# Optimization experiments

Hardware: AMD Instinct MI355X
Metric: run time of the kernel (lower is better)

## Reference

```python
import jax, jax.numpy as jnp
import numpy as np

N_HEADS = 4
M = 16            # n_points (neighbors kept per voxel)
DIST = 4          # manhattan distance threshold
D_MODEL = 128
D_FFN = 256
D_CHL = 64
GRID = 96         # spatial_shape per axis
LN_EPS = 1e-5
BN_EPS = 1e-3


def setup_inputs() -> dict:
    key = jax.random.key(0)
    ks = jax.random.split(key, 24)
    N = 8192
    w = lambda k, s: jax.random.normal(k, s, jnp.float32) * 0.02
    z = lambda d: jnp.zeros((d,), jnp.float32)
    o = lambda d: jnp.ones((d,), jnp.float32)
    return {
        "features": jax.random.normal(ks[0], (N, D_CHL), jnp.float32),
        "coords": jax.random.randint(ks[1], (N, 3), 0, GRID, jnp.int32),
        "pe_w1": w(ks[2], (3, D_MODEL // 2)), "pe_b1": z(D_MODEL // 2),
        "pe_w2": w(ks[3], (D_MODEL // 2, D_MODEL)), "pe_b2": z(D_MODEL),
        "in_w": w(ks[4], (D_CHL, D_MODEL)), "in_b": z(D_MODEL),
        "q_w": w(ks[5], (D_MODEL, D_MODEL)), "q_b": z(D_MODEL),
        "k_w": w(ks[6], (D_MODEL, D_MODEL)), "k_b": z(D_MODEL),
        "v_w": w(ks[7], (D_MODEL, D_MODEL)), "v_b": z(D_MODEL),
        "o_w": w(ks[8], (D_MODEL, D_MODEL)), "o_b": z(D_MODEL),
        "n1_g": o(D_MODEL), "n1_b": z(D_MODEL),
        "l1_w": w(ks[9], (D_MODEL, D_FFN)), "l1_b": z(D_FFN),
        "l2_w": w(ks[10], (D_FFN, D_MODEL)), "l2_b": z(D_MODEL),
        "n3_g": o(D_MODEL), "n3_b": z(D_MODEL),
        "fu_w": w(ks[11], (D_MODEL + D_CHL, D_CHL)), "fu_b": z(D_CHL),
        "bn_g": o(D_CHL), "bn_b": z(D_CHL),
    }


def _layernorm(x, g, b):
    mu = jnp.mean(x, -1, keepdims=True)
    var = jnp.mean(jnp.square(x - mu), -1, keepdims=True)
    return (x - mu) * jax.lax.rsqrt(var + LN_EPS) * g + b


def reference(features, coords, pe_w1, pe_b1, pe_w2, pe_b2, in_w, in_b,
              q_w, q_b, k_w, k_b, v_w, v_b, o_w, o_b, n1_g, n1_b,
              l1_w, l1_b, l2_w, l2_b, n3_g, n3_b, fu_w, fu_b, bn_g, bn_b):
    N = features.shape[0]
    hd = D_MODEL // N_HEADS
    ci = coords.astype(jnp.float32)
    # input projection + dynamic learnable positional encoding
    src = features @ in_w + in_b
    vc = ci / (GRID - 1.0)
    src = src + (jax.nn.relu(vc @ pe_w1 + pe_b1) @ pe_w2 + pe_b2)
    # pairwise manhattan distances; accumulate per coordinate to avoid [N,N,3]
    dist = jnp.zeros((N, N), jnp.float32)
    for d in range(3):
        dist = dist + jnp.abs(ci[:, d, None] - ci[None, :, d])
    dist = jnp.where(dist <= DIST, dist, jnp.inf)
    neg_top, idx = jax.lax.top_k(-dist, M)          # [N, M]
    valid = neg_top != -jnp.inf
    # gather neighbor features; invalid slots are zero (as in torch)
    nb = jnp.where(valid[:, :, None], src[jnp.where(valid, idx, 0)], 0.0)  # [N,M,D]
    # cross-attention: query is neighbor 0 (self). NOTE: faithful raw .view
    # reshape of [N,M,D] -> [N,H,M,hd] (interleaves neighbor/head axes as torch does)
    q = (nb[:, :1] @ q_w + q_b).reshape(N, N_HEADS, 1, hd)
    k = (nb @ k_w + k_b).reshape(N, N_HEADS, M, hd)
    v = (nb @ v_w + v_b).reshape(N, N_HEADS, M, hd)
    scores = jnp.einsum('nhqd,nhkd->nhqk', q, k) / jnp.sqrt(jnp.float32(D_MODEL))
    attn = jax.nn.softmax(scores, axis=-1)
    head_out = jnp.einsum('nhqk,nhkd->nhqd', attn, v).reshape(N, D_MODEL)
    out = head_out @ o_w + o_b
    tgt = _layernorm(src + out, n1_g, n1_b)
    # FFN
    tgt2 = jax.nn.relu(tgt @ l1_w + l1_b) @ l2_w + l2_b
    tgt = _layernorm(tgt + tgt2, n3_g, n3_b)
    # EnhancedFusion: concat -> linear -> batchnorm (train-mode stats) -> relu
    fused = jnp.concatenate([features, tgt], axis=1) @ fu_w + fu_b
    mu = jnp.mean(fused, 0)
    var = jnp.var(fused, 0)
    fused = (fused - mu) * jax.lax.rsqrt(var + BN_EPS) * bn_g + bn_b
    return jax.nn.relu(fused)
```

## Files before the change

### kernel.cpp

```cpp
#include <hip/hip_runtime.h>

#define DEVFN __device__ __forceinline__

DEVFN float relu(float x) { return x < 0.f ? 0.f : x; }

__global__ __launch_bounds__(256, 4) void ka_pre_cst(
    const float* __restrict__ features, const int* __restrict__ coords,
    const float* __restrict__ pe_w1, const float* __restrict__ pe_b1,
    const float* __restrict__ pe_w2, const float* __restrict__ pe_b2,
    const float* __restrict__ in_w, const float* __restrict__ in_b,
    const float* __restrict__ q_w, const float* __restrict__ k_w,
    const float* __restrict__ v_w,
    float* __restrict__ src,
    float* __restrict__ qs, float* __restrict__ ks, float* __restrict__ vs,
    int* __restrict__ nbr, float* __restrict__ bnAcc, int N)
{
    __shared__ float sF[512];
    __shared__ float sH[512];
    __shared__ float S[1024];
    __shared__ int   sC[24];
    __shared__ int cnt[16];
    __shared__ int lst[16 * 64];
    __shared__ int outL[256];

    const int tid = threadIdx.x;
    const int bx = blockIdx.x;
    const int role_nbr = (bx % 3) == 2;

    if (role_nbr) {
        const int nb = bx / 3;
        const int q0 = nb * 16;
        if (nb == 0 && tid < 128) bnAcc[tid] = 0.f;
        if (tid < 16) cnt[tid] = 0;
        outL[tid] = -1;
        __syncthreads();
        int qx[16], qy[16], qz[16];
#pragma unroll
        for (int q = 0; q < 16; ++q) {
            qx[q] = coords[(q0 + q) * 3 + 0];
            qy[q] = coords[(q0 + q) * 3 + 1];
            qz[q] = coords[(q0 + q) * 3 + 2];
        }
        for (int cd = tid; cd < N; cd += 256) {
            int cx = coords[cd * 3 + 0];
            int cy = coords[cd * 3 + 1];
            int cz = coords[cd * 3 + 2];
#pragma unroll
            for (int q = 0; q < 16; ++q) {
                int dx = cx - qx[q]; dx = dx < 0 ? -dx : dx;
                int dy = cy - qy[q]; dy = dy < 0 ? -dy : dy;
                int dz = cz - qz[q]; dz = dz < 0 ? -dz : dz;
                int d = dx + dy + dz;
                if (d <= 4) {
                    int s = atomicAdd(&cnt[q], 1);
                    if (s < 64) lst[q * 64 + s] = (d << 13) | cd;
                }
            }
        }
        __syncthreads();
        {
            const int q = tid >> 4, t = tid & 15;
            int n = cnt[q]; if (n > 64) n = 64;
            for (int e = t; e < n; e += 16) {
                int key = lst[q * 64 + e];
                int rank = 0;
                for (int j = 0; j < n; ++j) rank += (lst[q * 64 + j] < key) ? 1 : 0;
                if (rank < 16) outL[q * 16 + rank] = key & 8191;
            }
        }
        __syncthreads();
        {
            const int q = tid >> 4, t = tid & 15;
            nbr[(q0 + q) * 16 + t] = outL[q * 16 + t];
        }
        return;
    }

    const int sb = (bx / 3) * 2 + (bx % 3);
    const int r0 = sb * 8;
    if (tid < 24) sC[tid] = coords[r0 * 3 + tid];
    for (int i = tid; i < 512; i += 256) sF[i] = features[r0 * 64 + i];
    __syncthreads();
    for (int i = tid; i < 512; i += 256) {
        int r = i >> 6, t = i & 63;
        float v0 = sC[r * 3 + 0] * (1.f / 95.f);
        float v1 = sC[r * 3 + 1] * (1.f / 95.f);
        float v2 = sC[r * 3 + 2] * (1.f / 95.f);
        float h = v0 * pe_w1[t] + v1 * pe_w1[64 + t] + v2 * pe_w1[128 + t] + pe_b1[t];
        sH[i] = relu(h);
    }
    __syncthreads();
    const int c = tid & 127, rh = tid >> 7;
    {
        float acc[4];
        const float base = in_b[c] + pe_b2[c];
#pragma unroll
        for (int r = 0; r < 4; ++r) acc[r] = base;
        for (int j = 0; j < 64; ++j) {
            float w1 = in_w[j * 128 + c];
            float w2 = pe_w2[j * 128 + c];
#pragma unroll
            for (int r = 0; r < 4; ++r) {
                int rr = rh * 4 + r;
                acc[r] += sF[rr * 64 + j] * w1 + sH[rr * 64 + j] * w2;
            }
        }
#pragma unroll
        for (int r = 0; r < 4; ++r) {
            src[(r0 + rh * 4 + r) * 128 + c] = acc[r];
            S[(rh * 4 + r) * 128 + c] = acc[r];
        }
    }
    __syncthreads();
    {
        float aq[4], ak[4], av[4];
#pragma unroll
        for (int r = 0; r < 4; ++r) { aq[r] = 0.f; ak[r] = 0.f; av[r] = 0.f; }
        for (int k4 = 0; k4 < 32; ++k4) {
            float wq0 = q_w[(k4 * 4 + 0) * 128 + c];
            float wq1 = q_w[(k4 * 4 + 1) * 128 + c];
            float wq2 = q_w[(k4 * 4 + 2) * 128 + c];
            float wq3 = q_w[(k4 * 4 + 3) * 128 + c];
            float wk0 = k_w[(k4 * 4 + 0) * 128 + c];
            float wk1 = k_w[(k4 * 4 + 1) * 128 + c];
            float wk2 = k_w[(k4 * 4 + 2) * 128 + c];
            float wk3 = k_w[(k4 * 4 + 3) * 128 + c];
            float wv0 = v_w[(k4 * 4 + 0) * 128 + c];
            float wv1 = v_w[(k4 * 4 + 1) * 128 + c];
            float wv2 = v_w[(k4 * 4 + 2) * 128 + c];
            float wv3 = v_w[(k4 * 4 + 3) * 128 + c];
#pragma unroll
            for (int r = 0; r < 4; ++r) {
                float4 s = *(const float4*)(&S[(rh * 4 + r) * 128 + k4 * 4]);
                aq[r] += s.x * wq0 + s.y * wq1 + s.z * wq2 + s.w * wq3;
                ak[r] += s.x * wk0 + s.y * wk1 + s.z * wk2 + s.w * wk3;
                av[r] += s.x * wv0 + s.y * wv1 + s.z * wv2 + s.w * wv3;
            }
        }
#pragma unroll
        for (int r = 0; r < 4; ++r) {
            qs[(r0 + rh * 4 + r) * 128 + c] = aq[r];
            ks[(r0 + rh * 4 + r) * 128 + c] = ak[r];
            vs[(r0 + rh * 4 + r) * 128 + c] = av[r];
        }
    }
}

DEVFN void ln_rows8(float* Cb, const float* __restrict__ g,
                    const float* __restrict__ b, int tid)
{
    const int r = tid >> 5, l = tid & 31;
    float x[4]; float s = 0.f, s2 = 0.f;
#pragma unroll
    for (int i = 0; i < 4; ++i) {
        x[i] = Cb[r * 128 + l * 4 + i];
        s += x[i]; s2 += x[i] * x[i];
    }
#pragma unroll
    for (int o = 1; o < 32; o <<= 1) { s += __shfl_xor(s, o); s2 += __shfl_xor(s2, o); }
    float mu = s * (1.f / 128.f);
    float var = s2 * (1.f / 128.f) - mu * mu;
    float rstd = rsqrtf(var + 1e-5f);
#pragma unroll
    for (int i = 0; i < 4; ++i) {
        int cc = l * 4 + i;
        Cb[r * 128 + cc] = (x[i] - mu) * rstd * g[cc] + b[cc];
    }
}

__global__ __launch_bounds__(256, 4) void k4_main_cst(
    const float* __restrict__ features, const float* __restrict__ src,
    const float* __restrict__ qs, const float* __restrict__ ks, const float* __restrict__ vs,
    const int* __restrict__ nbr,
    const float* __restrict__ q_b, const float* __restrict__ k_b,
    const float* __restrict__ v_b,
    const float* __restrict__ o_w, const float* __restrict__ o_b,
    const float* __restrict__ n1_g, const float* __restrict__ n1_b,
    const float* __restrict__ l1_w, const float* __restrict__ l1_b,
    const float* __restrict__ l2_w, const float* __restrict__ l2_b,
    const float* __restrict__ n3_g, const float* __restrict__ n3_b,
    const float* __restrict__ fu_w, const float* __restrict__ fu_b,
    float* __restrict__ fused, float* __restrict__ bnSum, float* __restrict__ bnSq)
{
    __shared__ float A[1024];
    __shared__ float Bt[1024];
    __shared__ float C[1024];
    __shared__ float Q[1024];
    __shared__ float H[2048];
    __shared__ float SC[512];
    __shared__ float F[512];
    __shared__ __align__(16) float bK[128], bV[128];
    __shared__ int idxL[128];
    const int tid = threadIdx.x;
    const int r0 = blockIdx.x * 8;

    for (int i = tid; i < 1024; i += 256) A[i] = src[r0 * 128 + i];
    for (int i = tid; i < 512; i += 256) F[i] = features[r0 * 64 + i];
    if (tid < 128) {
        idxL[tid] = nbr[r0 * 16 + tid];
        bK[tid] = k_b[tid]; bV[tid] = v_b[tid];
    }
    __syncthreads();
    {
        int r = tid >> 5, cg = tid & 31;
        int i0 = idxL[r * 16];
        float4 qv = make_float4(0.f, 0.f, 0.f, 0.f);
        if (i0 >= 0) qv = *(const float4*)(qs + i0 * 128 + cg * 4);
        float4 qb = *(const float4*)(q_b + cg * 4);
        qv.x += qb.x; qv.y += qb.y; qv.z += qb.z; qv.w += qb.w;
        *(float4*)(&Q[r * 128 + cg * 4]) = qv;
    }
    __syncthreads();

    const int ar = tid >> 5, ah = (tid >> 3) & 3, ag = tid & 7;
    {
#pragma unroll
        for (int jj = 0; jj < 2; ++jj) {
            int j = ag + jj * 8;
            int j4 = j >> 2, ch = j & 3;
            int id = idxL[ar * 16 + ah * 4 + j4];
            float s = 0.f;
#pragma unroll
            for (int c4 = 0; c4 < 8; ++c4) {
                float4 qv = *(const float4*)(&Q[ar * 128 + ah * 32 + c4 * 4]);
                float4 kb = *(const float4*)(&bK[ch * 32 + c4 * 4]);
                float4 kv = make_float4(0.f, 0.f, 0.f, 0.f);
                if (id >= 0) kv = *(const float4*)(ks + id * 128 + ch * 32 + c4 * 4);
                s += qv.x * (kv.x + kb.x) + qv.y * (kv.y + kb.y)
                   + qv.z * (kv.z + kb.z) + qv.w * (kv.w + kb.w);
            }
            SC[ar * 64 + ah * 16 + j] = s * 0.08838834764831845f;
        }
    }
    __syncthreads();

    {
        float p[16];
        float mx = -3.4e38f;
#pragma unroll
        for (int j = 0; j < 16; ++j) { p[j] = SC[ar * 64 + ah * 16 + j]; mx = fmaxf(mx, p[j]); }
        float sum = 0.f;
#pragma unroll
        for (int j = 0; j < 16; ++j) { p[j] = __expf(p[j] - mx); sum += p[j]; }
        float inv = 1.f / sum;
        float4 acc = make_float4(0.f, 0.f, 0.f, 0.f);
#pragma unroll
        for (int j = 0; j < 16; ++j) {
            int j4 = j >> 2, ch = j & 3;
            int id = idxL[ar * 16 + ah * 4 + j4];
            float4 vb = *(const float4*)(&bV[ch * 32 + ag * 4]);
            float4 vv = make_float4(0.f, 0.f, 0.f, 0.f);
            if (id >= 0) vv = *(const float4*)(vs + id * 128 + ch * 32 + ag * 4);
            float w = p[j] * inv;
            acc.x += w * (vv.x + vb.x); acc.y += w * (vv.y + vb.y);
            acc.z += w * (vv.z + vb.z); acc.w += w * (vv.w + vb.w);
        }
        *(float4*)(&Bt[ar * 128 + ah * 32 + ag * 4]) = acc;
    }
    __syncthreads();

    {
        const int c = tid & 127, kh = tid >> 7;
        float acc[8];
#pragma unroll
        for (int r = 0; r < 8; ++r) acc[r] = 0.f;
        const float* wp = o_w + kh * 64 * 128 + c;
        for (int k4 = 0; k4 < 16; ++k4) {
            float w0 = wp[(k4 * 4 + 0) * 128];
            float w1 = wp[(k4 * 4 + 1) * 128];
            float w2 = wp[(k4 * 4 + 2) * 128];
            float w3 = wp[(k4 * 4 + 3) * 128];
#pragma unroll
            for (int r = 0; r < 8; ++r) {
                float4 t = *(const float4*)(&Bt[r * 128 + kh * 64 + k4 * 4]);
                acc[r] += t.x * w0 + t.y * w1 + t.z * w2 + t.w * w3;
            }
        }
#pragma unroll
        for (int r = 0; r < 8; ++r) H[kh * 1024 + r * 128 + c] = acc[r];
    }
    __syncthreads();
    for (int i = tid; i < 1024; i += 256) {
        int c = i & 127;
        C[i] = A[i] + o_b[c] + H[i] + H[1024 + i];
    }
    __syncthreads();
    ln_rows8(C, n1_g, n1_b, tid);
    __syncthreads();

    {
        const int f = tid;
        float acc[8];
#pragma unroll
        for (int r = 0; r < 8; ++r) acc[r] = 0.f;
        for (int k4 = 0; k4 < 32; ++k4) {
            float w0 = l1_w[(k4 * 4 + 0) * 256 + f];
            float w1 = l1_w[(k4 * 4 + 1) * 256 + f];
            float w2 = l1_w[(k4 * 4 + 2) * 256 + f];
            float w3 = l1_w[(k4 * 4 + 3) * 256 + f];
#pragma unroll
            for (int r = 0; r < 8; ++r) {
                float4 t = *(const float4*)(&C[r * 128 + k4 * 4]);
                acc[r] += t.x * w0 + t.y * w1 + t.z * w2 + t.w * w3;
            }
        }
        const float bb = l1_b[f];
#pragma unroll
        for (int r = 0; r < 8; ++r) H[r * 256 + f] = relu(acc[r] + bb);
    }
    __syncthreads();

    {
        const int c = tid & 127, kh = tid >> 7;
        float acc[8];
#pragma unroll
        for (int r = 0; r < 8; ++r) acc[r] = 0.f;
        const float* wp = l2_w + kh * 128 * 128 + c;
        for (int k4 = 0; k4 < 32; ++k4) {
            float w0 = wp[(k4 * 4 + 0) * 128];
            float w1 = wp[(k4 * 4 + 1) * 128];
            float w2 = wp[(k4 * 4 + 2) * 128];
            float w3 = wp[(k4 * 4 + 3) * 128];
#pragma unroll
            for (int r = 0; r < 8; ++r) {
                float4 t = *(const float4*)(&H[r * 256 + kh * 128 + k4 * 4]);
                acc[r] += t.x * w0 + t.y * w1 + t.z * w2 + t.w * w3;
            }
        }
        float* P = kh ? Bt : A;
#pragma unroll
        for (int r = 0; r < 8; ++r) P[r * 128 + c] = acc[r];
    }
    __syncthreads();
    for (int i = tid; i < 1024; i += 256) {
        int c = i & 127;
        C[i] += l2_b[c] + A[i] + Bt[i];
    }
    __syncthreads();
    ln_rows8(C, n3_g, n3_b, tid);
    __syncthreads();

    {
        const int c = tid & 63, rg = tid >> 6;
        float acc[2];
        const float fb = fu_b[c];
#pragma unroll
        for (int r = 0; r < 2; ++r) acc[r] = fb;
        for (int j4 = 0; j4 < 16; ++j4) {
            float w0 = fu_w[(j4 * 4 + 0) * 64 + c];
            float w1 = fu_w[(j4 * 4 + 1) * 64 + c];
            float w2 = fu_w[(j4 * 4 + 2) * 64 + c];
            float w3 = fu_w[(j4 * 4 + 3) * 64 + c];
#pragma unroll
            for (int r = 0; r < 2; ++r) {
                float4 t = *(const float4*)(&F[(rg * 2 + r) * 64 + j4 * 4]);
                acc[r] += t.x * w0 + t.y * w1 + t.z * w2 + t.w * w3;
            }
        }
        for (int j4 = 0; j4 < 32; ++j4) {
            float w0 = fu_w[(64 + j4 * 4 + 0) * 64 + c];
            float w1 = fu_w[(64 + j4 * 4 + 1) * 64 + c];
            float w2 = fu_w[(64 + j4 * 4 + 2) * 64 + c];
            float w3 = fu_w[(64 + j4 * 4 + 3) * 64 + c];
#pragma unroll
            for (int r = 0; r < 2; ++r) {
                float4 t = *(const float4*)(&C[(rg * 2 + r) * 128 + j4 * 4]);
                acc[r] += t.x * w0 + t.y * w1 + t.z * w2 + t.w * w3;
            }
        }
#pragma unroll
        for (int r = 0; r < 2; ++r) {
            int row = rg * 2 + r;
            float v = acc[r];
            fused[(r0 + row) * 64 + c] = v;
            H[row * 64 + c] = v;
        }
    }
    __syncthreads();
    if (tid < 64) {
        float s = 0.f, s2 = 0.f;
#pragma unroll
        for (int r = 0; r < 8; ++r) { float x = H[r * 64 + tid]; s += x; s2 += x * x; }
        atomicAdd(&bnSum[tid], s);
        atomicAdd(&bnSq[tid], s2);
    }
}

__global__ __launch_bounds__(256) void k5_bn_cst(
    const float* __restrict__ fused, const float* __restrict__ bnSum,
    const float* __restrict__ bnSq,
    const float* __restrict__ g, const float* __restrict__ b,
    float* __restrict__ out, int N)
{
    const int total = N * 64;
    const float invN = 1.f / (float)N;
    for (int i = blockIdx.x * 256 + threadIdx.x; i < total; i += gridDim.x * 256) {
        int c = i & 63;
        float mu = bnSum[c] * invN;
        float var = bnSq[c] * invN - mu * mu;
        float x = fused[i];
        float y = (x - mu) * rsqrtf(var + 1e-3f) * g[c] + b[c];
        out[i] = relu(y);
    }
}

extern "C" void kernel_launch(void* const* d_in, const int* in_sizes, int n_in,
                              void* d_out, int out_size, void* d_ws, size_t ws_size,
                              hipStream_t stream)
{
    const float* features = (const float*)d_in[0];
    const int*   coords   = (const int*)d_in[1];
    const float* pe_w1 = (const float*)d_in[2];
    const float* pe_b1 = (const float*)d_in[3];
    const float* pe_w2 = (const float*)d_in[4];
    const float* pe_b2 = (const float*)d_in[5];
    const float* in_w  = (const float*)d_in[6];
    const float* in_b  = (const float*)d_in[7];
    const float* q_w   = (const float*)d_in[8];
    const float* q_b   = (const float*)d_in[9];
    const float* k_w   = (const float*)d_in[10];
    const float* k_b   = (const float*)d_in[11];
    const float* v_w   = (const float*)d_in[12];
    const float* v_b   = (const float*)d_in[13];
    const float* o_w   = (const float*)d_in[14];
    const float* o_b   = (const float*)d_in[15];
    const float* n1_g  = (const float*)d_in[16];
    const float* n1_b  = (const float*)d_in[17];
    const float* l1_w  = (const float*)d_in[18];
    const float* l1_b  = (const float*)d_in[19];
    const float* l2_w  = (const float*)d_in[20];
    const float* l2_b  = (const float*)d_in[21];
    const float* n3_g  = (const float*)d_in[22];
    const float* n3_b  = (const float*)d_in[23];
    const float* fu_w  = (const float*)d_in[24];
    const float* fu_b  = (const float*)d_in[25];
    const float* bn_g  = (const float*)d_in[26];
    const float* bn_b  = (const float*)d_in[27];

    const int N = in_sizes[0] / 64;

    float* src   = (float*)d_ws;
    float* qs    = src + (size_t)N * 128;
    float* ks    = qs  + (size_t)N * 128;
    float* vs    = ks  + (size_t)N * 128;
    float* fused = vs  + (size_t)N * 128;
    int*   nbr    = (int*)(fused + (size_t)N * 64);
    float* bnSum  = (float*)(nbr + (size_t)N * 16);
    float* bnSq   = bnSum + 64;

    ka_pre_cst<<<N / 8 + N / 16, 256, 0, stream>>>(features, coords,
                                                   pe_w1, pe_b1, pe_w2, pe_b2,
                                                   in_w, in_b, q_w, k_w, v_w,
                                                   src, qs, ks, vs, nbr, bnSum, N);
    k4_main_cst<<<N / 8, 256, 0, stream>>>(features, src, qs, ks, vs, nbr,
                                           q_b, k_b, v_b, o_w, o_b, n1_g, n1_b,
                                           l1_w, l1_b, l2_w, l2_b, n3_g, n3_b,
                                           fu_w, fu_b, fused, bnSum, bnSq);
    k5_bn_cst<<<512, 256, 0, stream>>>(fused, bnSum, bnSq, bn_g, bn_b,
                                       (float*)d_out, N);
}
```

Measured before the change: 218.2 us.

## Retile dense GEMMs in main kernel to 4-column register tiles with split-K

Rewrites the o_w, l1_w and l2_w matmuls in the main per-8-row kernel. Each thread now computes a 4-column by 2-or-4-row float4 tile with vectorised weight loads, and the K dimension is split across thread groups whose partial sums are reduced through shared memory. The bias, residual and ReLU epilogues are fused into that reduction, which removes the separate elementwise passes and their barriers. The goal is fewer scalar global weight loads and more register reuse per shared-memory read, at the cost of extra shared-memory partial buffers and serialised reduction steps. It also disables unrolling on the fusion linear loops.

```diff
diff --git a/kernel.cpp b/kernel.cpp
--- a/kernel.cpp
+++ b/kernel.cpp
@@ -168,6 +168,17 @@
     }
 }
 
+DEVFN void op4(float4& acc, const float4 a,
+               const float4 w0, const float4 w1, const float4 w2, const float4 w3)
+{
+    acc.x += a.x * w0.x + a.y * w1.x + a.z * w2.x + a.w * w3.x;
+    acc.y += a.x * w0.y + a.y * w1.y + a.z * w2.y + a.w * w3.y;
+    acc.z += a.x * w0.z + a.y * w1.z + a.z * w2.z + a.w * w3.z;
+    acc.w += a.x * w0.w + a.y * w1.w + a.z * w2.w + a.w * w3.w;
+}
+DEVFN float4 f4add(float4 a, float4 b)
+{ return make_float4(a.x + b.x, a.y + b.y, a.z + b.z, a.w + b.w); }
+
 __global__ __launch_bounds__(256, 4) void k4_main_cst(
     const float* __restrict__ features, const float* __restrict__ src,
     const float* __restrict__ qs, const float* __restrict__ ks, const float* __restrict__ vs,
@@ -182,13 +193,13 @@
     const float* __restrict__ fu_w, const float* __restrict__ fu_b,
     float* __restrict__ fused, float* __restrict__ bnSum, float* __restrict__ bnSq)
 {
-    __shared__ float A[1024];
-    __shared__ float Bt[1024];
-    __shared__ float C[1024];
-    __shared__ float Q[1024];
-    __shared__ float H[2048];
-    __shared__ float SC[512];
-    __shared__ float F[512];
+    __shared__ __align__(16) float A[1024];
+    __shared__ __align__(16) float Bt[1024];
+    __shared__ __align__(16) float C[1024];
+    __shared__ __align__(16) float Q[1024];
+    __shared__ __align__(16) float H[2048];
+    __shared__ __align__(16) float SC[512];
+    __shared__ __align__(16) float F[512];
     __shared__ __align__(16) float bK[128], bV[128];
     __shared__ int idxL[128];
     const int tid = threadIdx.x;
@@ -260,83 +271,149 @@
     __syncthreads();
 
     {
-        const int c = tid & 127, kh = tid >> 7;
-        float acc[8];
-#pragma unroll
-        for (int r = 0; r < 8; ++r) acc[r] = 0.f;
-        const float* wp = o_w + kh * 64 * 128 + c;
-        for (int k4 = 0; k4 < 16; ++k4) {
-            float w0 = wp[(k4 * 4 + 0) * 128];
-            float w1 = wp[(k4 * 4 + 1) * 128];
-            float w2 = wp[(k4 * 4 + 2) * 128];
-            float w3 = wp[(k4 * 4 + 3) * 128];
-#pragma unroll
-            for (int r = 0; r < 8; ++r) {
-                float4 t = *(const float4*)(&Bt[r * 128 + kh * 64 + k4 * 4]);
-                acc[r] += t.x * w0 + t.y * w1 + t.z * w2 + t.w * w3;
-            }
-        }
-#pragma unroll
-        for (int r = 0; r < 8; ++r) H[kh * 1024 + r * 128 + c] = acc[r];
-    }
-    __syncthreads();
-    for (int i = tid; i < 1024; i += 256) {
-        int c = i & 127;
-        C[i] = A[i] + o_b[c] + H[i] + H[1024 + i];
-    }
-    __syncthreads();
+        const int cg = tid & 31, rp = (tid >> 5) & 3, kh = tid >> 7;
+        const int c0 = cg * 4, r0l = rp * 2, k0 = kh * 64;
+        float4 ac0 = make_float4(0.f, 0.f, 0.f, 0.f);
+        float4 ac1 = make_float4(0.f, 0.f, 0.f, 0.f);
+#pragma unroll 1
+        for (int s = 0; s < 16; ++s) {
+            const int kk = k0 + s * 4;
+            const float* wp = o_w + kk * 128 + c0;
+            float4 w0 = *(const float4*)(wp);
+            float4 w1 = *(const float4*)(wp + 128);
+            float4 w2 = *(const float4*)(wp + 256);
+            float4 w3 = *(const float4*)(wp + 384);
+            float4 a0 = *(const float4*)(&Bt[(r0l + 0) * 128 + kk]);
+            float4 a1 = *(const float4*)(&Bt[(r0l + 1) * 128 + kk]);
+            op4(ac0, a0, w0, w1, w2, w3);
+            op4(ac1, a1, w0, w1, w2, w3);
+        }
+        if (kh) {
+            *(float4*)(&H[(r0l + 0) * 128 + c0]) = ac0;
+            *(float4*)(&H[(r0l + 1) * 128 + c0]) = ac1;
+        }
+        __syncthreads();
+        if (kh == 0) {
+            float4 ob = *(const float4*)(o_b + c0);
+#pragma unroll
+            for (int r = 0; r < 2; ++r) {
+                const int base = (r0l + r) * 128 + c0;
+                float4 av = *(const float4*)(&A[base]);
+                float4 ph = *(const float4*)(&H[base]);
+                float4 me = r ? ac1 : ac0;
+                float4 cv;
+                cv.x = av.x + ob.x + me.x + ph.x;
+                cv.y = av.y + ob.y + me.y + ph.y;
+                cv.z = av.z + ob.z + me.z + ph.z;
+                cv.w = av.w + ob.w + me.w + ph.w;
+                *(float4*)(&C[base]) = cv;
+            }
+        }
+        __syncthreads();
+    }
     ln_rows8(C, n1_g, n1_b, tid);
     __syncthreads();
 
     {
-        const int f = tid;
-        float acc[8];
-#pragma unroll
-        for (int r = 0; r < 8; ++r) acc[r] = 0.f;
-        for (int k4 = 0; k4 < 32; ++k4) {
-            float w0 = l1_w[(k4 * 4 + 0) * 256 + f];
-            float w1 = l1_w[(k4 * 4 + 1) * 256 + f];
-            float w2 = l1_w[(k4 * 4 + 2) * 256 + f];
-            float w3 = l1_w[(k4 * 4 + 3) * 256 + f];
-#pragma unroll
-            for (int r = 0; r < 8; ++r) {
-                float4 t = *(const float4*)(&C[r * 128 + k4 * 4]);
-                acc[r] += t.x * w0 + t.y * w1 + t.z * w2 + t.w * w3;
-            }
-        }
-        const float bb = l1_b[f];
-#pragma unroll
-        for (int r = 0; r < 8; ++r) H[r * 256 + f] = relu(acc[r] + bb);
-    }
-    __syncthreads();
-
-    {
-        const int c = tid & 127, kh = tid >> 7;
-        float acc[8];
-#pragma unroll
-        for (int r = 0; r < 8; ++r) acc[r] = 0.f;
-        const float* wp = l2_w + kh * 128 * 128 + c;
-        for (int k4 = 0; k4 < 32; ++k4) {
-            float w0 = wp[(k4 * 4 + 0) * 128];
-            float w1 = wp[(k4 * 4 + 1) * 128];
-            float w2 = wp[(k4 * 4 + 2) * 128];
-            float w3 = wp[(k4 * 4 + 3) * 128];
-#pragma unroll
-            for (int r = 0; r < 8; ++r) {
-                float4 t = *(const float4*)(&H[r * 256 + kh * 128 + k4 * 4]);
-                acc[r] += t.x * w0 + t.y * w1 + t.z * w2 + t.w * w3;
-            }
-        }
-        float* P = kh ? Bt : A;
-#pragma unroll
-        for (int r = 0; r < 8; ++r) P[r * 128 + c] = acc[r];
-    }
-    __syncthreads();
-    for (int i = tid; i < 1024; i += 256) {
-        int c = i & 127;
-        C[i] += l2_b[c] + A[i] + Bt[i];
-    }
-    __syncthreads();
+        const int cg = tid & 63, rh = (tid >> 6) & 1, kh = tid >> 7;
+        const int c0 = cg * 4, r0l = rh * 4, k0 = kh * 64;
+        float4 ac0 = make_float4(0.f, 0.f, 0.f, 0.f);
+        float4 ac1 = make_float4(0.f, 0.f, 0.f, 0.f);
+        float4 ac2 = make_float4(0.f, 0.f, 0.f, 0.f);
+        float4 ac3 = make_float4(0.f, 0.f, 0.f, 0.f);
+#pragma unroll 1
+        for (int s = 0; s < 16; ++s) {
+            const int kk = k0 + s * 4;
+            const float* wp = l1_w + kk * 256 + c0;
+            float4 w0 = *(const float4*)(wp);
+            float4 w1 = *(const float4*)(wp + 256);
+            float4 w2 = *(const float4*)(wp + 512);
+            float4 w3 = *(const float4*)(wp + 768);
+            float4 a0 = *(const float4*)(&C[(r0l + 0) * 128 + kk]);
+            float4 a1 = *(const float4*)(&C[(r0l + 1) * 128 + kk]);
+            float4 a2 = *(const float4*)(&C[(r0l + 2) * 128 + kk]);
+            float4 a3 = *(const float4*)(&C[(r0l + 3) * 128 + kk]);
+            op4(ac0, a0, w0, w1, w2, w3);
+            op4(ac1, a1, w0, w1, w2, w3);
+            op4(ac2, a2, w0, w1, w2, w3);
+            op4(ac3, a3, w0, w1, w2, w3);
+        }
+        float* PS = rh ? Bt : A;
+        if (kh) {
+            *(float4*)(&PS[0 * 256 + c0]) = ac0;
+            *(float4*)(&PS[1 * 256 + c0]) = ac1;
+            *(float4*)(&PS[2 * 256 + c0]) = ac2;
+            *(float4*)(&PS[3 * 256 + c0]) = ac3;
+        }
+        __syncthreads();
+        if (kh == 0) {
+            float4 lb = *(const float4*)(l1_b + c0);
+#pragma unroll
+            for (int r = 0; r < 4; ++r) {
+                float4 p = *(const float4*)(&PS[r * 256 + c0]);
+                float4 me = (r == 0) ? ac0 : (r == 1) ? ac1 : (r == 2) ? ac2 : ac3;
+                float4 h;
+                h.x = relu(me.x + p.x + lb.x);
+                h.y = relu(me.y + p.y + lb.y);
+                h.z = relu(me.z + p.z + lb.z);
+                h.w = relu(me.w + p.w + lb.w);
+                *(float4*)(&H[(r0l + r) * 256 + c0]) = h;
+            }
+        }
+        __syncthreads();
+    }
+
+    {
+        const int cg = tid & 31, rh = (tid >> 5) & 1, kq = tid >> 6;
+        const int c0 = cg * 4, r0l = rh * 4, k0 = kq * 64;
+        float4 ac0 = make_float4(0.f, 0.f, 0.f, 0.f);
+        float4 ac1 = make_float4(0.f, 0.f, 0.f, 0.f);
+        float4 ac2 = make_float4(0.f, 0.f, 0.f, 0.f);
+        float4 ac3 = make_float4(0.f, 0.f, 0.f, 0.f);
+#pragma unroll 1
+        for (int s = 0; s < 16; ++s) {
+            const int kk = k0 + s * 4;
+            const float* wp = l2_w + kk * 128 + c0;
+            float4 w0 = *(const float4*)(wp);
+            float4 w1 = *(const float4*)(wp + 128);
+            float4 w2 = *(const float4*)(wp + 256);
+            float4 w3 = *(const float4*)(wp + 384);
+            float4 a0 = *(const float4*)(&H[(r0l + 0) * 256 + kk]);
+            float4 a1 = *(const float4*)(&H[(r0l + 1) * 256 + kk]);
+            float4 a2 = *(const float4*)(&H[(r0l + 2) * 256 + kk]);
+            float4 a3 = *(const float4*)(&H[(r0l + 3) * 256 + kk]);
+            op4(ac0, a0, w0, w1, w2, w3);
+            op4(ac1, a1, w0, w1, w2, w3);
+            op4(ac2, a2, w0, w1, w2, w3);
+            op4(ac3, a3, w0, w1, w2, w3);
+        }
+        if (kq) {
+            float* dst = (kq == 1) ? A : ((kq == 2) ? Bt : Q);
+            *(float4*)(&dst[(r0l + 0) * 128 + c0]) = ac0;
+            *(float4*)(&dst[(r0l + 1) * 128 + c0]) = ac1;
+            *(float4*)(&dst[(r0l + 2) * 128 + c0]) = ac2;
+            *(float4*)(&dst[(r0l + 3) * 128 + c0]) = ac3;
+        }
+        __syncthreads();
+        if (kq == 0) {
+            float4 lb = *(const float4*)(l2_b + c0);
+#pragma unroll
+            for (int r = 0; r < 4; ++r) {
+                const int base = (r0l + r) * 128 + c0;
+                float4 cv = *(const float4*)(&C[base]);
+                float4 me = (r == 0) ? ac0 : (r == 1) ? ac1 : (r == 2) ? ac2 : ac3;
+                float4 p0 = *(const float4*)(&A[base]);
+                float4 p1 = *(const float4*)(&Bt[base]);
+                float4 p2 = *(const float4*)(&Q[base]);
+                cv.x += lb.x + me.x + p0.x + p1.x + p2.x;
+                cv.y += lb.y + me.y + p0.y + p1.y + p2.y;
+                cv.z += lb.z + me.z + p0.z + p1.z + p2.z;
+                cv.w += lb.w + me.w + p0.w + p1.w + p2.w;
+                *(float4*)(&C[base]) = cv;
+            }
+        }
+        __syncthreads();
+    }
     ln_rows8(C, n3_g, n3_b, tid);
     __syncthreads();
 
@@ -346,22 +423,22 @@
         const float fb = fu_b[c];
 #pragma unroll
         for (int r = 0; r < 2; ++r) acc[r] = fb;
+        const float* wA = fu_w + c;
+#pragma unroll 1
         for (int j4 = 0; j4 < 16; ++j4) {
-            float w0 = fu_w[(j4 * 4 + 0) * 64 + c];
-            float w1 = fu_w[(j4 * 4 + 1) * 64 + c];
-            float w2 = fu_w[(j4 * 4 + 2) * 64 + c];
-            float w3 = fu_w[(j4 * 4 + 3) * 64 + c];
+            float w0 = wA[(j4 * 4 + 0) * 64], w1 = wA[(j4 * 4 + 1) * 64];
+            float w2 = wA[(j4 * 4 + 2) * 64], w3 = wA[(j4 * 4 + 3) * 64];
 #pragma unroll
             for (int r = 0; r < 2; ++r) {
                 float4 t = *(const float4*)(&F[(rg * 2 + r) * 64 + j4 * 4]);
                 acc[r] += t.x * w0 + t.y * w1 + t.z * w2 + t.w * w3;
             }
         }
+        const float* wB = fu_w + 64 * 64 + c;
+#pragma unroll 1
         for (int j4 = 0; j4 < 32; ++j4) {
-            float w0 = fu_w[(64 + j4 * 4 + 0) * 64 + c];
-            float w1 = fu_w[(64 + j4 * 4 + 1) * 64 + c];
-            float w2 = fu_w[(64 + j4 * 4 + 2) * 64 + c];
-            float w3 = fu_w[(64 + j4 * 4 + 3) * 64 + c];
+            float w0 = wB[(j4 * 4 + 0) * 64], w1 = wB[(j4 * 4 + 1) * 64];
+            float w2 = wB[(j4 * 4 + 2) * 64], w3 = wB[(j4 * 4 + 3) * 64];
 #pragma unroll
             for (int r = 0; r < 2; ++r) {
                 float4 t = *(const float4*)(&C[(rg * 2 + r) * 128 + j4 * 4]);
```

Result: slower. 230.6 us (+5.7%).

## Halve block size to 128 threads and give each thread more rows and columns

Applied to the files above, without the earlier changes.

Both the pre-pass and main kernels now launch 128-thread blocks. Each thread computes all 8 rows, or two output columns in the FFN, so the split-K partial sums and their shared-memory reduction passes are removed. Shared buffers are unioned to cut LDS footprint, and LayerNorm and the gathers use wider float4 accesses. The intent is more register-level reuse of weight loads and fewer barriers and reduction steps. In exchange, per-thread register pressure rises and fewer threads are available per block for latency hiding, notably in the O(N²) neighbor scan.

```diff
diff --git a/kernel.cpp b/kernel.cpp
--- a/kernel.cpp
+++ b/kernel.cpp
@@ -4,7 +4,7 @@
 
 DEVFN float relu(float x) { return x < 0.f ? 0.f : x; }
 
-__global__ __launch_bounds__(256, 4) void ka_pre_cst(
+__global__ __launch_bounds__(128, 3) void ka_pre_cst(
     const float* __restrict__ features, const int* __restrict__ coords,
     const float* __restrict__ pe_w1, const float* __restrict__ pe_b1,
     const float* __restrict__ pe_w2, const float* __restrict__ pe_b2,
@@ -15,9 +15,9 @@
     float* __restrict__ qs, float* __restrict__ ks, float* __restrict__ vs,
     int* __restrict__ nbr, float* __restrict__ bnAcc, int N)
 {
-    __shared__ float sF[512];
-    __shared__ float sH[512];
-    __shared__ float S[1024];
+    __shared__ __align__(16) float sF[512];
+    __shared__ __align__(16) float sH[512];
+    __shared__ __align__(16) float S[1024];
     __shared__ int   sC[24];
     __shared__ int cnt[16];
     __shared__ int lst[16 * 64];
@@ -32,7 +32,7 @@
         const int q0 = nb * 16;
         if (nb == 0 && tid < 128) bnAcc[tid] = 0.f;
         if (tid < 16) cnt[tid] = 0;
-        outL[tid] = -1;
+        for (int i = tid; i < 256; i += 128) outL[i] = -1;
         __syncthreads();
         int qx[16], qy[16], qz[16];
 #pragma unroll
@@ -41,7 +41,7 @@
             qy[q] = coords[(q0 + q) * 3 + 1];
             qz[q] = coords[(q0 + q) * 3 + 2];
         }
-        for (int cd = tid; cd < N; cd += 256) {
+        for (int cd = tid; cd < N; cd += 128) {
             int cx = coords[cd * 3 + 0];
             int cy = coords[cd * 3 + 1];
             int cz = coords[cd * 3 + 2];
@@ -59,9 +59,9 @@
         }
         __syncthreads();
         {
-            const int q = tid >> 4, t = tid & 15;
+            const int q = tid >> 3, t = tid & 7;
             int n = cnt[q]; if (n > 64) n = 64;
-            for (int e = t; e < n; e += 16) {
+            for (int e = t; e < n; e += 8) {
                 int key = lst[q * 64 + e];
                 int rank = 0;
                 for (int j = 0; j < n; ++j) rank += (lst[q * 64 + j] < key) ? 1 : 0;
@@ -69,19 +69,19 @@
             }
         }
         __syncthreads();
-        {
-            const int q = tid >> 4, t = tid & 15;
-            nbr[(q0 + q) * 16 + t] = outL[q * 16 + t];
+        for (int i = tid; i < 256; i += 128) {
+            int q = i >> 4, t = i & 15;
+            nbr[(q0 + q) * 16 + t] = outL[i];
         }
         return;
     }
 
-    const int sb = (bx / 3) * 2 + (bx % 3);
-    const int r0 = sb * 8;
+    const int sidx = (bx / 3) * 2 + (bx % 3);
+    const int r0 = sidx * 8;
     if (tid < 24) sC[tid] = coords[r0 * 3 + tid];
-    for (int i = tid; i < 512; i += 256) sF[i] = features[r0 * 64 + i];
-    __syncthreads();
-    for (int i = tid; i < 512; i += 256) {
+    for (int i = tid; i < 512; i += 128) sF[i] = features[r0 * 64 + i];
+    __syncthreads();
+    for (int i = tid; i < 512; i += 128) {
         int r = i >> 6, t = i & 63;
         float v0 = sC[r * 3 + 0] * (1.f / 95.f);
         float v1 = sC[r * 3 + 1] * (1.f / 95.f);
@@ -90,32 +90,40 @@
         sH[i] = relu(h);
     }
     __syncthreads();
-    const int c = tid & 127, rh = tid >> 7;
-    {
-        float acc[4];
+    const int c = tid;
+    {
+        float acc[8];
         const float base = in_b[c] + pe_b2[c];
 #pragma unroll
-        for (int r = 0; r < 4; ++r) acc[r] = base;
-        for (int j = 0; j < 64; ++j) {
-            float w1 = in_w[j * 128 + c];
-            float w2 = pe_w2[j * 128 + c];
-#pragma unroll
-            for (int r = 0; r < 4; ++r) {
-                int rr = rh * 4 + r;
-                acc[r] += sF[rr * 64 + j] * w1 + sH[rr * 64 + j] * w2;
-            }
-        }
-#pragma unroll
-        for (int r = 0; r < 4; ++r) {
-            src[(r0 + rh * 4 + r) * 128 + c] = acc[r];
-            S[(rh * 4 + r) * 128 + c] = acc[r];
-        }
-    }
-    __syncthreads();
-    {
-        float aq[4], ak[4], av[4];
-#pragma unroll
-        for (int r = 0; r < 4; ++r) { aq[r] = 0.f; ak[r] = 0.f; av[r] = 0.f; }
+        for (int r = 0; r < 8; ++r) acc[r] = base;
+        for (int j4 = 0; j4 < 16; ++j4) {
+            float i0 = in_w[(j4 * 4 + 0) * 128 + c];
+            float i1 = in_w[(j4 * 4 + 1) * 128 + c];
+            float i2 = in_w[(j4 * 4 + 2) * 128 + c];
+            float i3 = in_w[(j4 * 4 + 3) * 128 + c];
+            float p0 = pe_w2[(j4 * 4 + 0) * 128 + c];
+            float p1 = pe_w2[(j4 * 4 + 1) * 128 + c];
+            float p2 = pe_w2[(j4 * 4 + 2) * 128 + c];
+            float p3 = pe_w2[(j4 * 4 + 3) * 128 + c];
+#pragma unroll
+            for (int r = 0; r < 8; ++r) {
+                float4 f = *(const float4*)(&sF[r * 64 + j4 * 4]);
+                float4 h = *(const float4*)(&sH[r * 64 + j4 * 4]);
+                acc[r] += f.x * i0 + f.y * i1 + f.z * i2 + f.w * i3
+                        + h.x * p0 + h.y * p1 + h.z * p2 + h.w * p3;
+            }
+        }
+#pragma unroll
+        for (int r = 0; r < 8; ++r) {
+            src[(r0 + r) * 128 + c] = acc[r];
+            S[r * 128 + c] = acc[r];
+        }
+    }
+    __syncthreads();
+    {
+        float aq[8], ak[8], av[8];
+#pragma unroll
+        for (int r = 0; r < 8; ++r) { aq[r] = 0.f; ak[r] = 0.f; av[r] = 0.f; }
         for (int k4 = 0; k4 < 32; ++k4) {
             float wq0 = q_w[(k4 * 4 + 0) * 128 + c];
             float wq1 = q_w[(k4 * 4 + 1) * 128 + c];
@@ -130,45 +138,53 @@
             float wv2 = v_w[(k4 * 4 + 2) * 128 + c];
             float wv3 = v_w[(k4 * 4 + 3) * 128 + c];
 #pragma unroll
-            for (int r = 0; r < 4; ++r) {
-                float4 s = *(const float4*)(&S[(rh * 4 + r) * 128 + k4 * 4]);
+            for (int r = 0; r < 8; ++r) {
+                float4 s = *(const float4*)(&S[r * 128 + k4 * 4]);
                 aq[r] += s.x * wq0 + s.y * wq1 + s.z * wq2 + s.w * wq3;
                 ak[r] += s.x * wk0 + s.y * wk1 + s.z * wk2 + s.w * wk3;
                 av[r] += s.x * wv0 + s.y * wv1 + s.z * wv2 + s.w * wv3;
             }
         }
 #pragma unroll
-        for (int r = 0; r < 4; ++r) {
-            qs[(r0 + rh * 4 + r) * 128 + c] = aq[r];
-            ks[(r0 + rh * 4 + r) * 128 + c] = ak[r];
-            vs[(r0 + rh * 4 + r) * 128 + c] = av[r];
+        for (int r = 0; r < 8; ++r) {
+            qs[(r0 + r) * 128 + c] = aq[r];
+            ks[(r0 + r) * 128 + c] = ak[r];
+            vs[(r0 + r) * 128 + c] = av[r];
         }
     }
 }
 
-DEVFN void ln_rows8(float* Cb, const float* __restrict__ g,
-                    const float* __restrict__ b, int tid)
+DEVFN void ln_rows8_128(float* Cb, const float* __restrict__ g,
+                        const float* __restrict__ b, int tid)
 {
-    const int r = tid >> 5, l = tid & 31;
-    float x[4]; float s = 0.f, s2 = 0.f;
-#pragma unroll
-    for (int i = 0; i < 4; ++i) {
-        x[i] = Cb[r * 128 + l * 4 + i];
-        s += x[i]; s2 += x[i] * x[i];
-    }
-#pragma unroll
-    for (int o = 1; o < 32; o <<= 1) { s += __shfl_xor(s, o); s2 += __shfl_xor(s2, o); }
+    const int r = tid >> 4, l = tid & 15;
+    float4 x0 = *(const float4*)(&Cb[r * 128 + l * 8]);
+    float4 x1 = *(const float4*)(&Cb[r * 128 + l * 8 + 4]);
+    float s  = x0.x + x0.y + x0.z + x0.w + x1.x + x1.y + x1.z + x1.w;
+    float s2 = x0.x * x0.x + x0.y * x0.y + x0.z * x0.z + x0.w * x0.w
+             + x1.x * x1.x + x1.y * x1.y + x1.z * x1.z + x1.w * x1.w;
+#pragma unroll
+    for (int o = 1; o < 16; o <<= 1) { s += __shfl_xor(s, o); s2 += __shfl_xor(s2, o); }
     float mu = s * (1.f / 128.f);
     float var = s2 * (1.f / 128.f) - mu * mu;
     float rstd = rsqrtf(var + 1e-5f);
-#pragma unroll
-    for (int i = 0; i < 4; ++i) {
-        int cc = l * 4 + i;
-        Cb[r * 128 + cc] = (x[i] - mu) * rstd * g[cc] + b[cc];
-    }
+    const int cc = l * 8;
+    float4 g0 = *(const float4*)(g + cc), g1 = *(const float4*)(g + cc + 4);
+    float4 b0 = *(const float4*)(b + cc), b1 = *(const float4*)(b + cc + 4);
+    float4 y0, y1;
+    y0.x = (x0.x - mu) * rstd * g0.x + b0.x;
+    y0.y = (x0.y - mu) * rstd * g0.y + b0.y;
+    y0.z = (x0.z - mu) * rstd * g0.z + b0.z;
+    y0.w = (x0.w - mu) * rstd * g0.w + b0.w;
+    y1.x = (x1.x - mu) * rstd * g1.x + b1.x;
+    y1.y = (x1.y - mu) * rstd * g1.y + b1.y;
+    y1.z = (x1.z - mu) * rstd * g1.z + b1.z;
+    y1.w = (x1.w - mu) * rstd * g1.w + b1.w;
+    *(float4*)(&Cb[r * 128 + cc]) = y0;
+    *(float4*)(&Cb[r * 128 + cc + 4]) = y1;
 }
 
-__global__ __launch_bounds__(256, 4) void k4_main_cst(
+__global__ __launch_bounds__(128, 3) void k4_main_cst(
     const float* __restrict__ features, const float* __restrict__ src,
     const float* __restrict__ qs, const float* __restrict__ ks, const float* __restrict__ vs,
     const int* __restrict__ nbr,
@@ -182,205 +198,227 @@
     const float* __restrict__ fu_w, const float* __restrict__ fu_b,
     float* __restrict__ fused, float* __restrict__ bnSum, float* __restrict__ bnSq)
 {
-    __shared__ float A[1024];
-    __shared__ float Bt[1024];
-    __shared__ float C[1024];
-    __shared__ float Q[1024];
-    __shared__ float H[2048];
-    __shared__ float SC[512];
-    __shared__ float F[512];
-    __shared__ __align__(16) float bK[128], bV[128];
+    __shared__ __align__(16) float A[1024];
+    __shared__ __align__(16) float Bt[1024];
+    __shared__ __align__(16) float C[1024];
+    __shared__ __align__(16) float F[512];
+    __shared__ __align__(16) union UN {
+        struct { float Q[1024]; float SC[512]; float bK[128]; float bV[128]; } a;
+        float H[2048];
+    } U;
     __shared__ int idxL[128];
     const int tid = threadIdx.x;
     const int r0 = blockIdx.x * 8;
 
-    for (int i = tid; i < 1024; i += 256) A[i] = src[r0 * 128 + i];
-    for (int i = tid; i < 512; i += 256) F[i] = features[r0 * 64 + i];
-    if (tid < 128) {
-        idxL[tid] = nbr[r0 * 16 + tid];
-        bK[tid] = k_b[tid]; bV[tid] = v_b[tid];
-    }
-    __syncthreads();
-    {
-        int r = tid >> 5, cg = tid & 31;
+    for (int i = tid; i < 1024; i += 128) A[i] = src[r0 * 128 + i];
+    for (int i = tid; i < 512; i += 128) F[i] = features[r0 * 64 + i];
+    idxL[tid] = nbr[r0 * 16 + tid];
+    U.a.bK[tid] = k_b[tid]; U.a.bV[tid] = v_b[tid];
+    __syncthreads();
+    {
+        int r = tid >> 4, cg = tid & 15;
         int i0 = idxL[r * 16];
-        float4 qv = make_float4(0.f, 0.f, 0.f, 0.f);
-        if (i0 >= 0) qv = *(const float4*)(qs + i0 * 128 + cg * 4);
-        float4 qb = *(const float4*)(q_b + cg * 4);
-        qv.x += qb.x; qv.y += qb.y; qv.z += qb.z; qv.w += qb.w;
-        *(float4*)(&Q[r * 128 + cg * 4]) = qv;
-    }
-    __syncthreads();
-
-    const int ar = tid >> 5, ah = (tid >> 3) & 3, ag = tid & 7;
-    {
-#pragma unroll
-        for (int jj = 0; jj < 2; ++jj) {
-            int j = ag + jj * 8;
-            int j4 = j >> 2, ch = j & 3;
-            int id = idxL[ar * 16 + ah * 4 + j4];
-            float s = 0.f;
-#pragma unroll
-            for (int c4 = 0; c4 < 8; ++c4) {
-                float4 qv = *(const float4*)(&Q[ar * 128 + ah * 32 + c4 * 4]);
-                float4 kb = *(const float4*)(&bK[ch * 32 + c4 * 4]);
-                float4 kv = make_float4(0.f, 0.f, 0.f, 0.f);
-                if (id >= 0) kv = *(const float4*)(ks + id * 128 + ch * 32 + c4 * 4);
-                s += qv.x * (kv.x + kb.x) + qv.y * (kv.y + kb.y)
-                   + qv.z * (kv.z + kb.z) + qv.w * (kv.w + kb.w);
-            }
-            SC[ar * 64 + ah * 16 + j] = s * 0.08838834764831845f;
-        }
-    }
-    __syncthreads();
-
-    {
+        float4 qa = make_float4(0.f, 0.f, 0.f, 0.f), qb = qa;
+        if (i0 >= 0) {
+            qa = *(const float4*)(qs + i0 * 128 + cg * 8);
+            qb = *(const float4*)(qs + i0 * 128 + cg * 8 + 4);
+        }
+        float4 ba = *(const float4*)(q_b + cg * 8);
+        float4 bb = *(const float4*)(q_b + cg * 8 + 4);
+        qa.x += ba.x; qa.y += ba.y; qa.z += ba.z; qa.w += ba.w;
+        qb.x += bb.x; qb.y += bb.y; qb.z += bb.z; qb.w += bb.w;
+        *(float4*)(&U.a.Q[r * 128 + cg * 8]) = qa;
+        *(float4*)(&U.a.Q[r * 128 + cg * 8 + 4]) = qb;
+    }
+    __syncthreads();
+
+    const int ar = tid >> 4, ah = (tid >> 2) & 3;
+    {
+        const int ag = tid & 3;
+        int id[4];
+#pragma unroll
+        for (int jj = 0; jj < 4; ++jj) id[jj] = idxL[ar * 16 + ah * 4 + jj];
+        float s0 = 0.f, s1 = 0.f, s2 = 0.f, s3 = 0.f;
+#pragma unroll
+        for (int c4 = 0; c4 < 8; ++c4) {
+            float4 qv = *(const float4*)(&U.a.Q[ar * 128 + ah * 32 + c4 * 4]);
+            float4 kb = *(const float4*)(&U.a.bK[ag * 32 + c4 * 4]);
+            float4 kv;
+#pragma unroll
+            for (int jj = 0; jj < 4; ++jj) {
+                kv = make_float4(0.f, 0.f, 0.f, 0.f);
+                if (id[jj] >= 0) kv = *(const float4*)(ks + id[jj] * 128 + ag * 32 + c4 * 4);
+                float d = qv.x * (kv.x + kb.x) + qv.y * (kv.y + kb.y)
+                        + qv.z * (kv.z + kb.z) + qv.w * (kv.w + kb.w);
+                if (jj == 0) s0 += d; else if (jj == 1) s1 += d;
+                else if (jj == 2) s2 += d; else s3 += d;
+            }
+        }
+        const float sc = 0.08838834764831845f;
+        U.a.SC[ar * 64 + ah * 16 + 0 * 4 + ag] = s0 * sc;
+        U.a.SC[ar * 64 + ah * 16 + 1 * 4 + ag] = s1 * sc;
+        U.a.SC[ar * 64 + ah * 16 + 2 * 4 + ag] = s2 * sc;
+        U.a.SC[ar * 64 + ah * 16 + 3 * 4 + ag] = s3 * sc;
+    }
+    __syncthreads();
+
+    {
+        const int ag2 = tid & 3;
         float p[16];
         float mx = -3.4e38f;
 #pragma unroll
-        for (int j = 0; j < 16; ++j) { p[j] = SC[ar * 64 + ah * 16 + j]; mx = fmaxf(mx, p[j]); }
+        for (int j = 0; j < 16; ++j) { p[j] = U.a.SC[ar * 64 + ah * 16 + j]; mx = fmaxf(mx, p[j]); }
         float sum = 0.f;
 #pragma unroll
         for (int j = 0; j < 16; ++j) { p[j] = __expf(p[j] - mx); sum += p[j]; }
         float inv = 1.f / sum;
-        float4 acc = make_float4(0.f, 0.f, 0.f, 0.f);
+        float4 vb0[4], vb1[4];
+#pragma unroll
+        for (int ch = 0; ch < 4; ++ch) {
+            vb0[ch] = *(const float4*)(&U.a.bV[ch * 32 + ag2 * 8]);
+            vb1[ch] = *(const float4*)(&U.a.bV[ch * 32 + ag2 * 8 + 4]);
+        }
+        float4 a0 = make_float4(0.f, 0.f, 0.f, 0.f), a1 = a0;
 #pragma unroll
         for (int j = 0; j < 16; ++j) {
-            int j4 = j >> 2, ch = j & 3;
+            const int j4 = j >> 2, ch = j & 3;
             int id = idxL[ar * 16 + ah * 4 + j4];
-            float4 vb = *(const float4*)(&bV[ch * 32 + ag * 4]);
-            float4 vv = make_float4(0.f, 0.f, 0.f, 0.f);
-            if (id >= 0) vv = *(const float4*)(vs + id * 128 + ch * 32 + ag * 4);
+            float4 v0 = make_float4(0.f, 0.f, 0.f, 0.f), v1 = v0;
+            if (id >= 0) {
+                v0 = *(const float4*)(vs + id * 128 + ch * 32 + ag2 * 8);
+                v1 = *(const float4*)(vs + id * 128 + ch * 32 + ag2 * 8 + 4);
+            }
             float w = p[j] * inv;
-            acc.x += w * (vv.x + vb.x); acc.y += w * (vv.y + vb.y);
-            acc.z += w * (vv.z + vb.z); acc.w += w * (vv.w + vb.w);
-        }
-        *(float4*)(&Bt[ar * 128 + ah * 32 + ag * 4]) = acc;
-    }
-    __syncthreads();
-
-    {
-        const int c = tid & 127, kh = tid >> 7;
-        float acc[8];
-#pragma unroll
-        for (int r = 0; r < 8; ++r) acc[r] = 0.f;
-        const float* wp = o_w + kh * 64 * 128 + c;
-        for (int k4 = 0; k4 < 16; ++k4) {
-            float w0 = wp[(k4 * 4 + 0) * 128];
-            float w1 = wp[(k4 * 4 + 1) * 128];
-            float w2 = wp[(k4 * 4 + 2) * 128];
-            float w3 = wp[(k4 * 4 + 3) * 128];
-#pragma unroll
-            for (int r = 0; r < 8; ++r) {
-                float4 t = *(const float4*)(&Bt[r * 128 + kh * 64 + k4 * 4]);
-                acc[r] += t.x * w0 + t.y * w1 + t.z * w2 + t.w * w3;
-            }
-        }
-#pragma unroll
-        for (int r = 0; r < 8; ++r) H[kh * 1024 + r * 128 + c] = acc[r];
-    }
-    __syncthreads();
-    for (int i = tid; i < 1024; i += 256) {
-        int c = i & 127;
-        C[i] = A[i] + o_b[c] + H[i] + H[1024 + i];
-    }
-    __syncthreads();
-    ln_rows8(C, n1_g, n1_b, tid);
-    __syncthreads();
-
-    {
-        const int f = tid;
+            a0.x += w * (v0.x + vb0[ch].x); a0.y += w * (v0.y + vb0[ch].y);
+            a0.z += w * (v0.z + vb0[ch].z); a0.w += w * (v0.w + vb0[ch].w);
+            a1.x += w * (v1.x + vb1[ch].x); a1.y += w * (v1.y + vb1[ch].y);
+            a1.z += w * (v1.z + vb1[ch].z); a1.w += w * (v1.w + vb1[ch].w);
+        }
+        *(float4*)(&Bt[ar * 128 + ah * 32 + ag2 * 8]) = a0;
+        *(float4*)(&Bt[ar * 128 + ah * 32 + ag2 * 8 + 4]) = a1;
+    }
+    __syncthreads();
+
+    {
+        const int c = tid;
         float acc[8];
 #pragma unroll
         for (int r = 0; r < 8; ++r) acc[r] = 0.f;
         for (int k4 = 0; k4 < 32; ++k4) {
-            float w0 = l1_w[(k4 * 4 + 0) * 256 + f];
-            float w1 = l1_w[(k4 * 4 + 1) * 256 + f];
-            float w2 = l1_w[(k4 * 4 + 2) * 256 + f];
-            float w3 = l1_w[(k4 * 4 + 3) * 256 + f];
+            float w0 = o_w[(k4 * 4 + 0) * 128 + c];
+            float w1 = o_w[(k4 * 4 + 1) * 128 + c];
+            float w2 = o_w[(k4 * 4 + 2) * 128 + c];
+            float w3 = o_w[(k4 * 4 + 3) * 128 + c];
+#pragma unroll
+            for (int r = 0; r < 8; ++r) {
+                float4 t = *(const float4*)(&Bt[r * 128 + k4 * 4]);
+                acc[r] += t.x * w0 + t.y * w1 + t.z * w2 + t.w * w3;
+            }
+        }
+        const float ob = o_b[c];
+#pragma unroll
+        for (int r = 0; r < 8; ++r) C[r * 128 + c] = A[r * 128 + c] + ob + acc[r];
+    }
+    __syncthreads();
+    ln_rows8_128(C, n1_g, n1_b, tid);
+    __syncthreads();
+
+    {
+        const int c = tid;
+        float acc0[8], acc1[8];
+#pragma unroll
+        for (int r = 0; r < 8; ++r) { acc0[r] = 0.f; acc1[r] = 0.f; }
+        for (int k4 = 0; k4 < 32; ++k4) {
+            float a0 = l1_w[(k4 * 4 + 0) * 256 + c];
+            float a1 = l1_w[(k4 * 4 + 1) * 256 + c];
+            float a2 = l1_w[(k4 * 4 + 2) * 256 + c];
+            float a3 = l1_w[(k4 * 4 + 3) * 256 + c];
+            float b0 = l1_w[(k4 * 4 + 0) * 256 + c + 128];
+            float b1 = l1_w[(k4 * 4 + 1) * 256 + c + 128];
+            float b2 = l1_w[(k4 * 4 + 2) * 256 + c + 128];
+            float b3 = l1_w[(k4 * 4 + 3) * 256 + c + 128];
 #pragma unroll
             for (int r = 0; r < 8; ++r) {
                 float4 t = *(const float4*)(&C[r * 128 + k4 * 4]);
+                acc0[r] += t.x * a0 + t.y * a1 + t.z * a2 + t.w * a3;
+                acc1[r] += t.x * b0 + t.y * b1 + t.z * b2 + t.w * b3;
+            }
+        }
+        const float lb0 = l1_b[c], lb1 = l1_b[c + 128];
+#pragma unroll
+        for (int r = 0; r < 8; ++r) {
+            U.H[r * 256 + c]       = relu(acc0[r] + lb0);
+            U.H[r * 256 + c + 128] = relu(acc1[r] + lb1);
+        }
+    }
+    __syncthreads();
+
+    {
+        const int c = tid;
+        float acc[8];
+#pragma unroll
+        for (int r = 0; r < 8; ++r) acc[r] = 0.f;
+        for (int k4 = 0; k4 < 64; ++k4) {
+            float w0 = l2_w[(k4 * 4 + 0) * 128 + c];
+            float w1 = l2_w[(k4 * 4 + 1) * 128 + c];
+            float w2 = l2_w[(k4 * 4 + 2) * 128 + c];
+            float w3 = l2_w[(k4 * 4 + 3) * 128 + c];
+#pragma unroll
+            for (int r = 0; r < 8; ++r) {
+                float4 t = *(const float4*)(&U.H[r * 256 + k4 * 4]);
                 acc[r] += t.x * w0 + t.y * w1 + t.z * w2 + t.w * w3;
             }
         }
-        const float bb = l1_b[f];
-#pragma unroll
-        for (int r = 0; r < 8; ++r) H[r * 256 + f] = relu(acc[r] + bb);
-    }
-    __syncthreads();
-
-    {
-        const int c = tid & 127, kh = tid >> 7;
-        float acc[8];
-#pragma unroll
-        for (int r = 0; r < 8; ++r) acc[r] = 0.f;
-        const float* wp = l2_w + kh * 128 * 128 + c;
-        for (int k4 = 0; k4 < 32; ++k4) {
-            float w0 = wp[(k4 * 4 + 0) * 128];
-            float w1 = wp[(k4 * 4 + 1) * 128];
-            float w2 = wp[(k4 * 4 + 2) * 128];
-            float w3 = wp[(k4 * 4 + 3) * 128];
-#pragma unroll
-            for (int r = 0; r < 8; ++r) {
-                float4 t = *(const float4*)(&H[r * 256 + kh * 128 + k4 * 4]);
-                acc[r] += t.x * w0 + t.y * w1 + t.z * w2 + t.w * w3;
-            }
-        }
-        float* P = kh ? Bt : A;
-#pragma unroll
-        for (int r = 0; r < 8; ++r) P[r * 128 + c] = acc[r];
-    }
-    __syncthreads();
-    for (int i = tid; i < 1024; i += 256) {
-        int c = i & 127;
-        C[i] += l2_b[c] + A[i] + Bt[i];
-    }
-    __syncthreads();
-    ln_rows8(C, n3_g, n3_b, tid);
-    __syncthreads();
-
-    {
-        const int c = tid & 63, rg = tid >> 6;
-        float acc[2];
+        const float lb = l2_b[c];
+#pragma unroll
+        for (int r = 0; r < 8; ++r) C[r * 128 + c] += lb + acc[r];
+    }
+    __syncthreads();
+    ln_rows8_128(C, n3_g, n3_b, tid);
+    __syncthreads();
+
+    {
+        const int c = tid & 63, rh = tid >> 6;
+        float acc[4];
         const float fb = fu_b[c];
 #pragma unroll
-        for (int r = 0; r < 2; ++r) acc[r] = fb;
+        for (int r = 0; r < 4; ++r) acc[r] = fb;
         for (int j4 = 0; j4 < 16; ++j4) {
             float w0 = fu_w[(j4 * 4 + 0) * 64 + c];
             float w1 = fu_w[(j4 * 4 + 1) * 64 + c];
             float w2 = fu_w[(j4 * 4 + 2) * 64 + c];
             float w3 = fu_w[(j4 * 4 + 3) * 64 + c];
 #pragma unroll
-            for (int r = 0; r < 2; ++r) {
-                float4 t = *(const float4*)(&F[(rg * 2 + r) * 64 + j4 * 4]);
+            for (int r = 0; r < 4; ++r) {
+                float4 t = *(const float4*)(&F[(rh * 4 + r) * 64 + j4 * 4]);
                 acc[r] += t.x * w0 + t.y * w1 + t.z * w2 + t.w * w3;
             }
         }
+        const float* wB = fu_w + 64 * 64;
         for (int j4 = 0; j4 < 32; ++j4) {
-            float w0 = fu_w[(64 + j4 * 4 + 0) * 64 + c];
-            float w1 = fu_w[(64 + j4 * 4 + 1) * 64 + c];
-            float w2 = fu_w[(64 + j4 * 4 + 2) * 64 + c];
-            float w3 = fu_w[(64 + j4 * 4 + 3) * 64 + c];
-#pragma unroll
-            for (int r = 0; r < 2; ++r) {
-                float4 t = *(const float4*)(&C[(rg * 2 + r) * 128 + j4 * 4]);
+            float w0 = wB[(j4 * 4 + 0) * 64 + c];
+            float w1 = wB[(j4 * 4 + 1) * 64 + c];
+            float w2 = wB[(j4 * 4 + 2) * 64 + c];
+            float w3 = wB[(j4 * 4 + 3) * 64 + c];
+#pragma unroll
+            for (int r = 0; r < 4; ++r) {
+                float4 t = *(const float4*)(&C[(rh * 4 + r) * 128 + j4 * 4]);
                 acc[r] += t.x * w0 + t.y * w1 + t.z * w2 + t.w * w3;
             }
         }
 #pragma unroll
-        for (int r = 0; r < 2; ++r) {
-            int row = rg * 2 + r;
+        for (int r = 0; r < 4; ++r) {
+            int row = rh * 4 + r;
             float v = acc[r];
             fused[(r0 + row) * 64 + c] = v;
-            H[row * 64 + c] = v;
+            A[row * 64 + c] = v;
         }
     }
     __syncthreads();
     if (tid < 64) {
         float s = 0.f, s2 = 0.f;
 #pragma unroll
-        for (int r = 0; r < 8; ++r) { float x = H[r * 64 + tid]; s += x; s2 += x * x; }
+        for (int r = 0; r < 8; ++r) { float x = A[r * 64 + tid]; s += x; s2 += x * x; }
         atomicAdd(&bnSum[tid], s);
         atomicAdd(&bnSq[tid], s2);
     }
@@ -448,11 +486,11 @@
     float* bnSum  = (float*)(nbr + (size_t)N * 16);
     float* bnSq   = bnSum + 64;
 
-    ka_pre_cst<<<N / 8 + N / 16, 256, 0, stream>>>(features, coords,
+    ka_pre_cst<<<N / 8 + N / 16, 128, 0, stream>>>(features, coords,
                                                    pe_w1, pe_b1, pe_w2, pe_b2,
                                                    in_w, in_b, q_w, k_w, v_w,
                                                    src, qs, ks, vs, nbr, bnSum, N);
-    k4_main_cst<<<N / 8, 256, 0, stream>>>(features, src, qs, ks, vs, nbr,
+    k4_main_cst<<<N / 8, 128, 0, stream>>>(features, src, qs, ks, vs, nbr,
                                            q_b, k_b, v_b, o_w, o_b, n1_g, n1_b,
                                            l1_w, l1_b, l2_w, l2_b, n3_g, n3_b,
                                            fu_w, fu_b, fused, bnSum, bnSq);
```

Result: slower. 259.7 us (+19.0%).
